# Optimization experiments

Hardware: AMD Instinct MI355X
Metric: run time of the kernel (lower is better)

Reference implementation:

```python
import jax, jax.numpy as jnp
import numpy as np
import math

N_HEADS, D_MODEL, D_HEAD = 16, 1024, 64
INIT_RANGE = 0.02


def setup_inputs() -> dict:
    key = jax.random.key(0)
    ks = jax.random.split(key, 5)
    x = jax.random.normal(ks[0], (2, 2048, D_MODEL), dtype=jnp.float32)
    W_Q = INIT_RANGE * jax.random.normal(ks[1], (N_HEADS, D_MODEL, D_HEAD), dtype=jnp.float32)
    W_K = INIT_RANGE * jax.random.normal(ks[2], (N_HEADS, D_MODEL, D_HEAD), dtype=jnp.float32)
    W_V = INIT_RANGE * jax.random.normal(ks[3], (N_HEADS, D_MODEL, D_HEAD), dtype=jnp.float32)
    W_O = INIT_RANGE * jax.random.normal(ks[4], (N_HEADS, D_HEAD, D_MODEL), dtype=jnp.float32)
    b_Q = jnp.zeros((N_HEADS, D_HEAD), jnp.float32)
    b_K = jnp.zeros((N_HEADS, D_HEAD), jnp.float32)
    b_V = jnp.zeros((N_HEADS, D_HEAD), jnp.float32)
    b_O = jnp.zeros((D_MODEL,), jnp.float32)
    return {"x": x, "W_Q": W_Q, "W_K": W_K, "W_V": W_V, "W_O": W_O,
            "b_Q": b_Q, "b_K": b_K, "b_V": b_V, "b_O": b_O}


def reference(x, W_Q, W_K, W_V, W_O, b_Q, b_K, b_V, b_O):
    # x: [b, p, d_model]
    Q = jnp.einsum('ndh,bpd->bpnh', W_Q, x) + b_Q  # [b, p, n, h]
    K = jnp.einsum('ndh,bpd->bpnh', W_K, x) + b_K
    V = jnp.einsum('ndh,bpd->bpnh', W_V, x) + b_V
    scores = jnp.einsum('bqnh,bknh->bnqk', Q, K) / math.sqrt(D_HEAD)  # [b, n, pq, pk]
    S = scores.shape[-1]
    causal_mask = jnp.triu(jnp.ones((S, S), dtype=bool), k=1)  # True above diag -> masked
    scores = jnp.where(causal_mask, -jnp.inf, scores)
    pattern = jax.nn.softmax(scores, axis=-1)  # [b, n, pq, pk]
    z = jnp.einsum('bnqk,bknh->bqnh', pattern, V)  # [b, pq, n, h]
    attn_out = jnp.einsum('bqnh,nhd->bqd', z, W_O) + b_O  # [b, pq, d_model]
    return attn_out
```

## Files before the change

kernel.cpp:

```cpp
#include <hip/hip_runtime.h>
#include <hip/hip_bf16.h>

#define DI __device__ __forceinline__

using f32x4  = __attribute__((ext_vector_type(4)))  float;
using f32x16 = __attribute__((ext_vector_type(16))) float;
using s16x8  = __attribute__((ext_vector_type(8)))  short;
using s32x4  = __attribute__((ext_vector_type(4)))  int;
using u16x4  = __attribute__((ext_vector_type(4)))  unsigned short;
using u32x4  = __attribute__((ext_vector_type(4)))  unsigned;

typedef __attribute__((address_space(3))) unsigned       lds_u32;
typedef __attribute__((address_space(3))) unsigned short lds_u16;
typedef const __attribute__((address_space(1))) unsigned ga_u32;

DI unsigned short f2bf(float f) {
  union { float f; unsigned u; } v; v.f = f;
  unsigned r = v.u + 0x7FFFu + ((v.u >> 16) & 1u);
  return (unsigned short)(r >> 16);
}

DI unsigned cvtpk(float lo, float hi) {
  unsigned d;
  asm("v_cvt_pk_bf16_f32 %0, %1, %2" : "=v"(d) : "v"(lo), "v"(hi));
  return d;
}
DI void pswap(unsigned &a, unsigned &b) {
  asm("v_permlane32_swap_b32 %0, %1" : "+v"(a), "+v"(b));
}

#define QSCALE 0.18033688011112042f

__global__ void k_prep(const float* __restrict__ x, const float* __restrict__ wq,
                       const float* __restrict__ wk, const float* __restrict__ wv,
                       const float* __restrict__ wo, unsigned short* __restrict__ xb,
                       unsigned short* __restrict__ Wt, unsigned short* __restrict__ Wot) {
  int bid = blockIdx.x;
  if (bid < 4096) {
    int i = (bid * 256 + threadIdx.x) * 4;
    f32x4 v = *reinterpret_cast<const f32x4*>(x + i);
    u16x4 o;
    o[0] = f2bf(v[0]); o[1] = f2bf(v[1]); o[2] = f2bf(v[2]); o[3] = f2bf(v[3]);
    *reinterpret_cast<u16x4*>(xb + i) = o;
  } else if (bid < 16384) {
    int o = (bid - 4096) * 256 + threadIdx.x;
    int k = o & 1023, h = (o >> 10) & 63, n = (o >> 16) & 15, w = o >> 20;
    const float* W = (w == 0) ? wq : (w == 1) ? wk : wv;
    Wt[o] = f2bf(W[(n * 1024 + k) * 64 + h]);
  } else {
    int o = (bid - 16384) * 256 + threadIdx.x;
    int k = o & 1023, d = o >> 10;
    Wot[o] = f2bf(wo[k * 1024 + d]);
  }
}

template <int MODE, int BM>
__launch_bounds__(256, 3)
__global__ void k_gemm(const unsigned short* __restrict__ A,
                       const unsigned short* __restrict__ Bt,
                       const float* __restrict__ bq, const float* __restrict__ bk,
                       const float* __restrict__ bv, const float* __restrict__ bo,
                       unsigned short* __restrict__ oq, unsigned short* __restrict__ ok_,
                       unsigned short* __restrict__ ov, float* __restrict__ of) {
  constexpr int MFR = BM / 32;
  __shared__ __align__(16) unsigned short As[BM * 64];
  __shared__ __align__(16) unsigned short Bs[128 * 64];
  const int t = threadIdx.x;
  const int lane = t & 63, wid = t >> 6;
  const int wm = wid >> 1, wn = wid & 1;
  const int l15 = lane & 15, l4 = lane >> 4;
  const int m0 = blockIdx.y * BM, c0 = blockIdx.x * 128;

  f32x4 acc[MFR][4] = {};

  for (int k0 = 0; k0 < 1024; k0 += 64) {
    if (k0) __syncthreads();
    {
      const int r_l = lane >> 3, kb = lane & 7;
#pragma unroll
      for (int i = 0; i < MFR; ++i) {
        int rbase = wid * (BM / 4) + i * 8;
        int r = rbase + r_l;
        int ksrc = (kb ^ (r & 7)) * 8;
        __builtin_amdgcn_global_load_lds(
            (ga_u32*)(A + (long)(m0 + r) * 1024 + k0 + ksrc),
            (lds_u32*)((lds_u16*)As + rbase * 64), 16, 0, 0);
      }
#pragma unroll
      for (int i = 0; i < 4; ++i) {
        int rbase = wid * 32 + i * 8;
        int r = rbase + r_l;
        int ksrc = (kb ^ (r & 7)) * 8;
        __builtin_amdgcn_global_load_lds(
            (ga_u32*)(Bt + (long)(c0 + r) * 1024 + k0 + ksrc),
            (lds_u32*)((lds_u16*)Bs + rbase * 64), 16, 0, 0);
      }
    }
    __syncthreads();
    s16x8 af[MFR][2], bf[4][2];
#pragma unroll
    for (int mb = 0; mb < MFR; ++mb) {
      int r = wm * (BM / 2) + mb * 16 + l15;
#pragma unroll
      for (int kc = 0; kc < 2; ++kc) {
        int byo = (kc * 64 + l4 * 16) ^ ((r & 7) << 4);
        af[mb][kc] = *reinterpret_cast<const s16x8*>(&As[r * 64 + (byo >> 1)]);
      }
    }
#pragma unroll
    for (int nb = 0; nb < 4; ++nb) {
      int r = wn * 64 + nb * 16 + l15;
#pragma unroll
      for (int kc = 0; kc < 2; ++kc) {
        int byo = (kc * 64 + l4 * 16) ^ ((r & 7) << 4);
        bf[nb][kc] = *reinterpret_cast<const s16x8*>(&Bs[r * 64 + (byo >> 1)]);
      }
    }
#pragma unroll
    for (int mb = 0; mb < MFR; ++mb)
#pragma unroll
      for (int nb = 0; nb < 4; ++nb) {
        acc[mb][nb] = __builtin_amdgcn_mfma_f32_16x16x32_bf16(af[mb][0], bf[nb][0], acc[mb][nb], 0, 0, 0);
        acc[mb][nb] = __builtin_amdgcn_mfma_f32_16x16x32_bf16(af[mb][1], bf[nb][1], acc[mb][nb], 0, 0, 0);
      }
  }

#pragma unroll
  for (int mb = 0; mb < MFR; ++mb) {
#pragma unroll
    for (int nb = 0; nb < 4; ++nb) {
      int c = c0 + wn * 64 + nb * 16 + l15;
      int mbase = m0 + wm * (BM / 2) + mb * 16 + l4 * 4;
      if (MODE == 0) {
        int w = c >> 10, cc = c & 1023;
        int nH = cc >> 6, h = cc & 63;
        const float* bias = (w == 0) ? bq : (w == 1) ? bk : bv;
        float bval = bias[cc];
        if (w == 2) {
          int bb = mbase >> 11, p = mbase & 2047;
          u16x4 pk4;
#pragma unroll
          for (int r = 0; r < 4; ++r) pk4[r] = f2bf(acc[mb][nb][r] + bval);
          *reinterpret_cast<u16x4*>(ov + (((long)bb * 16 + nH) * 64 + h) * 2048 + p) = pk4;
        } else {
          unsigned short* dst = (w == 0) ? oq : ok_;
          float scl = (w == 0) ? QSCALE : 1.0f;
#pragma unroll
          for (int r = 0; r < 4; ++r) {
            int m = mbase + r;
            int bb = m >> 11, p = m & 2047;
            dst[(((long)bb * 16 + nH) * 2048 + p) * 64 + h] = f2bf((acc[mb][nb][r] + bval) * scl);
          }
        }
      } else {
#pragma unroll
        for (int r = 0; r < 4; ++r) of[(long)(mbase + r) * 1024 + c] = acc[mb][nb][r] + bo[c];
      }
    }
  }
}

__launch_bounds__(256, 2)
__global__ void k_attn(const unsigned short* __restrict__ Q,
                       const unsigned short* __restrict__ K,
                       const unsigned short* __restrict__ VT,
                       unsigned short* __restrict__ Z) {
  __shared__ __align__(16) unsigned short KV[2][2 * 128 * 64];
  const int t = threadIdx.x;
  const int lane = t & 63, wv = t >> 6;
  const int l31 = lane & 31, h5 = lane >> 5;
  const int id = blockIdx.x;
  const int xcd = id & 7, j = id >> 3;
  const int bn = (j & 3) * 8 + xcd;
  const int qt = 15 - (j >> 2);
  const int b = bn >> 4, n = bn & 15;
  const int r0w = qt * 128 + wv * 32;
  const int qq = r0w + l31;
  const int nkt = qt + 1;
  const unsigned short* Qb = Q + (long)bn * (2048 * 64);
  const unsigned short* Kb = K + (long)bn * (2048 * 64);
  const unsigned short* Vb = VT + (long)bn * (64 * 2048);
  unsigned* Zd = (unsigned*)Z;
  const int swl  = (l31 & 7) << 4;
  const int swlV = (l31 & 15) << 4;

  auto stage = [&](int k0s, int nb) {
    const int rl = lane >> 3, cl = lane & 7;
#pragma unroll
    for (int i = 0; i < 4; ++i) {
      int rbase = wv * 32 + i * 8;
      int r = rbase + rl;
      __builtin_amdgcn_global_load_lds(
          (ga_u32*)(Kb + (long)(k0s + r) * 64 + ((cl ^ (r & 7)) * 8)),
          (lds_u32*)((lds_u16*)&KV[nb][0] + rbase * 64), 16, 0, 0);
    }
    const int rv = lane >> 4, sl = lane & 15;
#pragma unroll
    for (int i = 0; i < 4; ++i) {
      int rbase = wv * 16 + i * 4;
      int hr = rbase + rv;
      __builtin_amdgcn_global_load_lds(
          (ga_u32*)(Vb + (long)hr * 2048 + k0s + ((sl ^ (hr & 15)) * 8)),
          (lds_u32*)((lds_u16*)&KV[nb][128 * 64] + rbase * 128), 16, 0, 0);
    }
  };

  s16x8 qf[4];
#pragma unroll
  for (int hc = 0; hc < 4; ++hc)
    qf[hc] = *reinterpret_cast<const s16x8*>(Qb + (long)qq * 64 + hc * 16 + h5 * 8);

  f32x16 o0 = {}, o1 = {};
  float lrun = 0.f;

  stage(0, 0);

  for (int kt = 0; kt < nkt; ++kt) {
    const int k0 = kt << 7;
    const int cb = kt & 1;
    __syncthreads();
    if (kt + 1 < nkt) stage((kt + 1) << 7, cb ^ 1);
    const unsigned short* Ks = &KV[cb][0];
    const unsigned short* Vs = &KV[cb][128 * 64];
    const bool last = (kt == nkt - 1);
    const int kbmax = last ? wv : 3;

    f32x16 s[4] = {};
    __builtin_amdgcn_s_setprio(1);
#pragma unroll
    for (int kb = 0; kb < 4; ++kb) {
      if (kb > kbmax) continue;
#pragma unroll
      for (int hc = 0; hc < 4; ++hc) {
        int cbk = hc * 32 + h5 * 16;
        s16x8 kf = *reinterpret_cast<const s16x8*>(
            &Ks[(kb * 32 + l31) * 64 + ((cbk ^ swl) >> 1)]);
        s[kb] = __builtin_amdgcn_mfma_f32_32x32x16_bf16(kf, qf[hc], s[kb], 0, 0, 0);
      }
    }
    __builtin_amdgcn_s_setprio(0);

    if (last) {
#pragma unroll
      for (int kb = 0; kb < 4; ++kb) {
        if (kb != wv) continue;
#pragma unroll
        for (int r = 0; r < 16; ++r) {
          int kA = k0 + kb * 32 + (r & 3) + 8 * (r >> 2) + 4 * h5;
          if (kA > qq) s[kb][r] = -1e30f;
        }
      }
    }

    float rs = 0.f;
#pragma unroll
    for (int kb = 0; kb < 4; ++kb) {
      if (kb > kbmax) continue;
#pragma unroll
      for (int r = 0; r < 16; ++r) { s[kb][r] = __builtin_exp2f(s[kb][r]); rs += s[kb][r]; }
    }
    rs += __shfl_xor(rs, 32);
    lrun += rs;

    __builtin_amdgcn_s_setprio(1);
#pragma unroll
    for (int kb = 0; kb < 4; ++kb) {
      if (kb > kbmax) continue;
      unsigned PK[8];
#pragma unroll
      for (int m2 = 0; m2 < 8; ++m2) PK[m2] = cvtpk(s[kb][2 * m2], s[kb][2 * m2 + 1]);
#pragma unroll
      for (int cl2 = 0; cl2 < 2; ++cl2) {
        int base = cl2 * 4;
        unsigned x0 = PK[base + 0], y0 = PK[base + 2];
        unsigned x1 = PK[base + 1], y1 = PK[base + 3];
        pswap(x0, y0);
        pswap(x1, y1);
        union { s32x4 i; s16x8 h; } u2;
        u2.i = s32x4{(int)x0, (int)x1, (int)y0, (int)y1};
        int c = kb * 2 + cl2;
        int cbv = c * 32 + h5 * 16;
        s16x8 vf0 = *reinterpret_cast<const s16x8*>(&Vs[l31 * 128 + ((cbv ^ swlV) >> 1)]);
        s16x8 vf1 = *reinterpret_cast<const s16x8*>(&Vs[(32 + l31) * 128 + ((cbv ^ swlV) >> 1)]);
        o0 = __builtin_amdgcn_mfma_f32_32x32x16_bf16(vf0, u2.h, o0, 0, 0, 0);
        o1 = __builtin_amdgcn_mfma_f32_32x32x16_bf16(vf1, u2.h, o1, 0, 0, 0);
      }
    }
    __builtin_amdgcn_s_setprio(0);
  }

  __syncthreads();
  unsigned* Zl = reinterpret_cast<unsigned*>(&KV[0][0]) + wv * (32 * 33);
  float inv = 1.0f / lrun;
#pragma unroll
  for (int hb = 0; hb < 2; ++hb) {
#pragma unroll
    for (int rp = 0; rp < 8; ++rp) {
      float vlo = (hb ? o1[2 * rp] : o0[2 * rp]) * inv;
      float vhi = (hb ? o1[2 * rp + 1] : o0[2 * rp + 1]) * inv;
      unsigned d = cvtpk(vlo, vhi);
      int col = 16 * hb + 4 * (rp >> 1) + 2 * h5 + (rp & 1);
      Zl[l31 * 33 + col] = d;
    }
  }
  asm volatile("s_waitcnt lgkmcnt(0)" ::: "memory");
  const int qr = lane >> 1, cbs = (lane & 1) * 16;
  const long zb = ((long)(b * 2048 + r0w + qr)) * 512 + n * 32;
#pragma unroll
  for (int c2 = 0; c2 < 4; ++c2) {
    u32x4 w4;
#pragma unroll
    for (int i2 = 0; i2 < 4; ++i2) w4[i2] = Zl[qr * 33 + cbs + 4 * c2 + i2];
    *reinterpret_cast<u32x4*>(Zd + zb + cbs + 4 * c2) = w4;
  }
}

extern "C" void kernel_launch(void* const* d_in, const int* in_sizes, int n_in,
                              void* d_out, int out_size, void* d_ws, size_t ws_size,
                              hipStream_t stream) {
  const float* x  = (const float*)d_in[0];
  const float* wq = (const float*)d_in[1];
  const float* wk = (const float*)d_in[2];
  const float* wv = (const float*)d_in[3];
  const float* wo = (const float*)d_in[4];
  const float* bq = (const float*)d_in[5];
  const float* bk = (const float*)d_in[6];
  const float* bv = (const float*)d_in[7];
  const float* bo = (const float*)d_in[8];
  char* ws = (char*)d_ws;
  unsigned short* xb  = (unsigned short*)(ws);
  unsigned short* Wt  = (unsigned short*)(ws + (8  << 20));
  unsigned short* Wot = (unsigned short*)(ws + (14 << 20));
  unsigned short* Qw  = (unsigned short*)(ws + (16 << 20));
  unsigned short* Kw  = (unsigned short*)(ws + (24 << 20));
  unsigned short* Vw  = (unsigned short*)(ws + (32 << 20));
  unsigned short* Zw  = (unsigned short*)(ws + (40 << 20));
  float* out = (float*)d_out;

  k_prep<<<20480, 256, 0, stream>>>(x, wq, wk, wv, wo, xb, Wt, Wot);
  k_gemm<0, 128><<<dim3(24, 32), 256, 0, stream>>>(xb, Wt, bq, bk, bv, nullptr,
                                                   Qw, Kw, Vw, nullptr);
  k_attn<<<512, 256, 0, stream>>>(Qw, Kw, Vw, Zw);
  k_gemm<1, 64><<<dim3(8, 64), 256, 0, stream>>>(Zw, Wot, nullptr, nullptr, nullptr, bo,
                                                 nullptr, nullptr, nullptr, out);
}
```

Before: 114.0 us.

## Tile weight transposes through LDS and compute softmax row sums with MFMA

The weight-prep kernel now transposes W_Q/K/V and W_O in 64x64 tiles staged through shared memory. This replaces strided, uncoalesced per-element global reads and shrinks the grid from 20480 to 5120 blocks. In attention, the per-row softmax denominator is now accumulated by an extra MFMA against a ones vector, using the same bf16-rounded probabilities, instead of scalar VALU adds plus a cross-lane shuffle. The extra MFMA adds matrix-core work per tile in exchange for fewer VALU ops and a denominator consistent with the P·V product.

```diff
diff --git a/kernel.cpp b/kernel.cpp
--- a/kernel.cpp
+++ b/kernel.cpp
@@ -35,22 +35,49 @@
                        const float* __restrict__ wk, const float* __restrict__ wv,
                        const float* __restrict__ wo, unsigned short* __restrict__ xb,
                        unsigned short* __restrict__ Wt, unsigned short* __restrict__ Wot) {
-  int bid = blockIdx.x;
+  __shared__ unsigned short Tl[64][66];
+  const int bid = blockIdx.x;
+  const int t = threadIdx.x;
   if (bid < 4096) {
-    int i = (bid * 256 + threadIdx.x) * 4;
+    int i = (bid * 256 + t) * 4;
     f32x4 v = *reinterpret_cast<const f32x4*>(x + i);
     u16x4 o;
     o[0] = f2bf(v[0]); o[1] = f2bf(v[1]); o[2] = f2bf(v[2]); o[3] = f2bf(v[3]);
     *reinterpret_cast<u16x4*>(xb + i) = o;
-  } else if (bid < 16384) {
-    int o = (bid - 4096) * 256 + threadIdx.x;
-    int k = o & 1023, h = (o >> 10) & 63, n = (o >> 16) & 15, w = o >> 20;
+  } else if (bid < 4096 + 768) {
+    int b2 = bid - 4096;
+    int w = b2 >> 8, n = (b2 >> 4) & 15, k0 = (b2 & 15) * 64;
     const float* W = (w == 0) ? wq : (w == 1) ? wk : wv;
-    Wt[o] = f2bf(W[(n * 1024 + k) * 64 + h]);
+    int h = t & 63, r4 = t >> 6;
+#pragma unroll
+    for (int i = 0; i < 16; ++i) {
+      int r = i * 4 + r4;
+      Tl[r][h] = f2bf(W[(n * 1024 + k0 + r) * 64 + h]);
+    }
+    __syncthreads();
+    int k = t & 63, h4 = t >> 6;
+    unsigned short* dst = Wt + (long)((w * 16 + n) * 64) * 1024 + k0;
+#pragma unroll
+    for (int i = 0; i < 16; ++i) {
+      int hh = i * 4 + h4;
+      dst[hh * 1024 + k] = Tl[k][hh];
+    }
   } else {
-    int o = (bid - 16384) * 256 + threadIdx.x;
-    int k = o & 1023, d = o >> 10;
-    Wot[o] = f2bf(wo[k * 1024 + d]);
+    int b3 = bid - 4096 - 768;
+    int d0 = (b3 >> 4) * 64, k0 = (b3 & 15) * 64;
+    int h = t & 63, r4 = t >> 6;
+#pragma unroll
+    for (int i = 0; i < 16; ++i) {
+      int r = i * 4 + r4;
+      Tl[r][h] = f2bf(wo[(k0 + r) * 1024 + d0 + h]);
+    }
+    __syncthreads();
+    int k = t & 63, h4 = t >> 6;
+#pragma unroll
+    for (int i = 0; i < 16; ++i) {
+      int hh = i * 4 + h4;
+      Wot[(long)(d0 + hh) * 1024 + k0 + k] = Tl[k][hh];
+    }
   }
 }
 
@@ -210,8 +237,12 @@
   for (int hc = 0; hc < 4; ++hc)
     qf[hc] = *reinterpret_cast<const s16x8*>(Qb + (long)qq * 64 + hc * 16 + h5 * 8);
 
+  s16x8 ones;
+#pragma unroll
+  for (int j2 = 0; j2 < 8; ++j2) ones[j2] = (short)0x3F80;
+
   f32x16 o0 = {}, o1 = {};
-  float lrun = 0.f;
+  f32x16 acc_l = {};
 
   stage(0, 0);
 
@@ -252,15 +283,12 @@
       }
     }
 
-    float rs = 0.f;
 #pragma unroll
     for (int kb = 0; kb < 4; ++kb) {
       if (kb > kbmax) continue;
 #pragma unroll
-      for (int r = 0; r < 16; ++r) { s[kb][r] = __builtin_exp2f(s[kb][r]); rs += s[kb][r]; }
-    }
-    rs += __shfl_xor(rs, 32);
-    lrun += rs;
+      for (int r = 0; r < 16; ++r) s[kb][r] = __builtin_exp2f(s[kb][r]);
+    }
 
     __builtin_amdgcn_s_setprio(1);
 #pragma unroll
@@ -284,6 +312,7 @@
         s16x8 vf1 = *reinterpret_cast<const s16x8*>(&Vs[(32 + l31) * 128 + ((cbv ^ swlV) >> 1)]);
         o0 = __builtin_amdgcn_mfma_f32_32x32x16_bf16(vf0, u2.h, o0, 0, 0, 0);
         o1 = __builtin_amdgcn_mfma_f32_32x32x16_bf16(vf1, u2.h, o1, 0, 0, 0);
+        acc_l = __builtin_amdgcn_mfma_f32_32x32x16_bf16(ones, u2.h, acc_l, 0, 0, 0);
       }
     }
     __builtin_amdgcn_s_setprio(0);
@@ -291,7 +320,7 @@
 
   __syncthreads();
   unsigned* Zl = reinterpret_cast<unsigned*>(&KV[0][0]) + wv * (32 * 33);
-  float inv = 1.0f / lrun;
+  float inv = 1.0f / acc_l[0];
 #pragma unroll
   for (int hb = 0; hb < 2; ++hb) {
 #pragma unroll
@@ -337,7 +366,7 @@
   unsigned short* Zw  = (unsigned short*)(ws + (40 << 20));
   float* out = (float*)d_out;
 
-  k_prep<<<20480, 256, 0, stream>>>(x, wq, wk, wv, wo, xb, Wt, Wot);
+  k_prep<<<5120, 256, 0, stream>>>(x, wq, wk, wv, wo, xb, Wt, Wot);
   k_gemm<0, 128><<<dim3(24, 32), 256, 0, stream>>>(xb, Wt, bq, bk, bv, nullptr,
                                                    Qw, Kw, Vw, nullptr);
   k_attn<<<512, 256, 0, stream>>>(Qw, Kw, Vw, Zw);
```

Result: faster. 103.3 us (-9.4%).
